# Performance work log

Hardware: AMD Instinct MI355X
Metric: run time of the kernel (lower is better)

Reference implementation:

```python
import jax, jax.numpy as jnp
import numpy as np

BATCH, SEQ_LEN, VEC_DIM, WIDTH = 64, 256, 512, 3


def setup_inputs() -> dict:
    key = jax.random.key(0)
    k = jax.random.split(key, 8)
    F0r = jax.random.normal(k[0], (BATCH, SEQ_LEN, VEC_DIM), jnp.float32)
    F1r = jax.random.normal(k[1], (BATCH, SEQ_LEN, VEC_DIM), jnp.float32)
    sent0_mask = (jax.random.uniform(k[2], (BATCH, SEQ_LEN)) < 0.9).astype(jnp.float32)
    sent1_mask = (jax.random.uniform(k[3], (BATCH, SEQ_LEN)) < 0.9).astype(jnp.float32)
    # nn.Parameter(torch.randn(seq_len, vec_dim))
    W0 = jax.random.normal(k[4], (SEQ_LEN, VEC_DIM), jnp.float32)
    W1 = jax.random.normal(k[5], (SEQ_LEN, VEC_DIM), jnp.float32)
    # Conv2d(2, 1, kernel_size=(WIDTH, 1)) default init: U(-1/sqrt(fan_in), +)
    bound = 1.0 / np.sqrt(2 * WIDTH * 1)
    conv_w = jax.random.uniform(k[6], (1, 2, WIDTH, 1), jnp.float32, -bound, bound)
    conv_b = jax.random.uniform(k[7], (1,), jnp.float32, -bound, bound)
    return dict(F0r=F0r, F1r=F1r, sent0_mask=sent0_mask, sent1_mask=sent1_mask,
                W0=W0, W1=W1, conv_w=conv_w, conv_b=conv_b)


def _conv_tanh_pool(x, conv_w, conv_b):
    # x: [B, 2, S, D]; conv pad (WIDTH-1, 0) -> [B, 1, S+WIDTH-1, D]
    y = jax.lax.conv_general_dilated(
        x, conv_w, window_strides=(1, 1),
        padding=((WIDTH - 1, WIDTH - 1), (0, 0)),
        dimension_numbers=('NCHW', 'OIHW', 'NCHW'))
    y = jnp.tanh(y + conv_b[None, :, None, None])
    # AvgPool2d kernel (WIDTH,1), stride 1 -> [B, 1, S, D]
    y = jax.lax.reduce_window(y, 0.0, jax.lax.add,
                              (1, 1, WIDTH, 1), (1, 1, 1, 1), 'VALID') / WIDTH
    return y[:, 0]  # squeeze channel -> [B, S, D]


def reference(F0r, F1r, sent0_mask, sent1_mask, W0, W1, conv_w, conv_b):
    # masking is in-place in the torch code, so masked F0/F1 feed the conv too
    F0 = F0r * sent0_mask[:, :, None]  # [B, S, D]
    F1 = F1r * sent1_mask[:, :, None]
    # pairwise L2 via ||u-v||^2 = ||u||^2 + ||v||^2 - 2 u.v (avoids [B,S,S,D])
    sq0 = jnp.sum(F0 * F0, axis=-1)  # [B, S]
    sq1 = jnp.sum(F1 * F1, axis=-1)
    cross = jnp.einsum('bid,bjd->bij', F0, F1)  # [B, S, S]
    d2 = jnp.maximum(sq0[:, :, None] + sq1[:, None, :] - 2.0 * cross, 0.0)
    norm = jnp.where(d2 > 0, jnp.sqrt(jnp.where(d2 > 0, d2, 1.0)), 0.0)
    A = 1.0 / (1.0 + norm)  # [B, S, S]
    F0a = jnp.einsum('bij,id->bjd', A, W0)  # A^T @ W0
    F1a = jnp.einsum('bij,jd->bid', A, W1)  # A @ W1
    x0 = jnp.stack([F0, F0a], axis=1)  # [B, 2, S, D]
    x1 = jnp.stack([F1, F1a], axis=1)
    out0 = _conv_tanh_pool(x0, conv_w, conv_b)
    out1 = _conv_tanh_pool(x1, conv_w, conv_b)
    return out0, out1
```

## Files before the change

### kernel.cpp

```cpp
#include <hip/hip_runtime.h>

typedef unsigned short u16;
typedef __attribute__((ext_vector_type(8))) short short8;
typedef __attribute__((ext_vector_type(4))) float f32x4;

__device__ inline u16 f2bf(float f) {
    union { float f; unsigned u; } v; v.f = f;
    unsigned u = v.u;
    unsigned r = (u + 0x7FFFu + ((u >> 16) & 1u)) >> 16;
    return (u16)r;
}
__device__ inline float bf2f(u16 h) {
    union { unsigned u; float f; } v; v.u = ((unsigned)h) << 16;
    return v.f;
}
__device__ inline float ftanh(float x) {
    float e = __expf(2.f * x);
    return 1.f - 2.f / (e + 1.f);
}

__global__ __launch_bounds__(128) void prep_kernel(
    const float* __restrict__ F0r, const float* __restrict__ F1r,
    const float* __restrict__ m0, const float* __restrict__ m1,
    const float* __restrict__ W0, const float* __restrict__ W1,
    u16* __restrict__ F0b, u16* __restrict__ F1b,
    u16* __restrict__ WT0, u16* __restrict__ WT1,
    float* __restrict__ sq0, float* __restrict__ sq1)
{
    int bx = blockIdx.x;
    int t = threadIdx.x;
    if (bx >= 16384) {
        int idx = (bx - 16384) * 128 + t;
        int a = idx >> 17;
        int r = idx & 131071;
        int s = r >> 9, d = r & 511;
        const float* W = a ? W1 : W0;
        u16* WT = a ? WT1 : WT0;
        WT[d * 256 + s] = f2bf(W[r]);
        return;
    }
    int bs = bx;
    size_t base = (size_t)bs * 512 + t * 4;
    float mk0 = m0[bs], mk1 = m1[bs];
    float4 v0 = *(const float4*)(F0r + base);
    float4 v1 = *(const float4*)(F1r + base);
    v0.x *= mk0; v0.y *= mk0; v0.z *= mk0; v0.w *= mk0;
    v1.x *= mk1; v1.y *= mk1; v1.z *= mk1; v1.w *= mk1;
    ushort4 u0; u0.x = f2bf(v0.x); u0.y = f2bf(v0.y); u0.z = f2bf(v0.z); u0.w = f2bf(v0.w);
    ushort4 u1; u1.x = f2bf(v1.x); u1.y = f2bf(v1.y); u1.z = f2bf(v1.z); u1.w = f2bf(v1.w);
    *(ushort4*)(F0b + base) = u0;
    *(ushort4*)(F1b + base) = u1;
    float s0p = v0.x*v0.x + v0.y*v0.y + v0.z*v0.z + v0.w*v0.w;
    float s1p = v1.x*v1.x + v1.y*v1.y + v1.z*v1.z + v1.w*v1.w;
    #pragma unroll
    for (int off = 32; off > 0; off >>= 1) {
        s0p += __shfl_xor(s0p, off);
        s1p += __shfl_xor(s1p, off);
    }
    __shared__ float red0[2], red1[2];
    if ((t & 63) == 0) { red0[t >> 6] = s0p; red1[t >> 6] = s1p; }
    __syncthreads();
    if (t == 0) { sq0[bs] = red0[0] + red0[1]; sq1[bs] = red1[0] + red1[1]; }
}

__global__ __launch_bounds__(256) void gemm_cross_kernel(
    const u16* __restrict__ F0b, const u16* __restrict__ F1b,
    const float* __restrict__ sq0, const float* __restrict__ sq1,
    u16* __restrict__ Abf, u16* __restrict__ ATbf)
{
    __shared__ __align__(16) u16 smem[64 * 136 * 2];
    u16 (*As)[136] = (u16(*)[136])smem;
    u16 (*Bs)[136] = (u16(*)[136])(smem + 64 * 136);

    int b = blockIdx.y;
    int i0 = (blockIdx.x >> 2) * 64, j0 = (blockIdx.x & 3) * 64;
    const u16* Ap = F0b + (size_t)b * 131072;
    const u16* Bp = F1b + (size_t)b * 131072;
    const float* sqR = sq0 + b * 256;
    const float* sqC = sq1 + b * 256;

    const int t = threadIdx.x;
    const int lane = t & 63, w = t >> 6;
    const int wm = w >> 1, wn = w & 1;
    const int q = lane >> 4, lm = lane & 15;

    f32x4 acc[2][2];
    #pragma unroll
    for (int x = 0; x < 2; ++x)
        #pragma unroll
        for (int y = 0; y < 2; ++y)
            acc[x][y] = (f32x4){0.f, 0.f, 0.f, 0.f};

    for (int k0 = 0; k0 < 512; k0 += 128) {
        #pragma unroll
        for (int i = 0; i < 4; ++i) {
            int idx = i * 256 + t;
            int row = idx >> 4;
            int seg = idx & 15;
            *(uint4*)&As[row][seg * 8] =
                *(const uint4*)(Ap + (size_t)(i0 + row) * 512 + k0 + seg * 8);
            *(uint4*)&Bs[row][seg * 8] =
                *(const uint4*)(Bp + (size_t)(j0 + row) * 512 + k0 + seg * 8);
        }
        __syncthreads();
        #pragma unroll
        for (int ks = 0; ks < 128; ks += 32) {
            short8 af[2], bfr[2];
            #pragma unroll
            for (int x = 0; x < 2; ++x) {
                af[x]  = *(const short8*)&As[wm * 32 + x * 16 + lm][ks + q * 8];
                bfr[x] = *(const short8*)&Bs[wn * 32 + x * 16 + lm][ks + q * 8];
            }
            #pragma unroll
            for (int x = 0; x < 2; ++x)
                #pragma unroll
                for (int y = 0; y < 2; ++y)
                    acc[x][y] = __builtin_amdgcn_mfma_f32_16x16x32_bf16(
                        af[x], bfr[y], acc[x][y], 0, 0, 0);
        }
        __syncthreads();
    }

    u16 (*Ct)[136] = (u16(*)[136])smem;
    #pragma unroll
    for (int x = 0; x < 2; ++x) {
        #pragma unroll
        for (int r = 0; r < 4; ++r) {
            int ir = wm * 32 + x * 16 + q * 4 + r;
            float si = sqR[i0 + ir];
            #pragma unroll
            for (int y = 0; y < 2; ++y) {
                int jc = wn * 32 + y * 16 + lm;
                float d2 = si + sqC[j0 + jc] - 2.f * acc[x][y][r];
                d2 = fmaxf(d2, 0.f);
                float a = 1.f / (1.f + sqrtf(d2));
                Ct[ir][jc] = f2bf(a);
            }
        }
    }
    __syncthreads();

    u16* Aout  = Abf  + (size_t)b * 65536;
    u16* ATout = ATbf + (size_t)b * 65536;
    int ii = t >> 2;
    int c0 = (t & 3) * 16;
    #pragma unroll
    for (int c = 0; c < 4; ++c) {
        ushort4 v = *(ushort4*)&Ct[ii][c0 + c * 4];
        *(ushort4*)&Aout[(size_t)(i0 + ii) * 256 + j0 + c0 + c * 4] = v;
    }
    #pragma unroll
    for (int c = 0; c < 4; ++c) {
        ushort4 v;
        v.x = Ct[c0 + c * 4 + 0][ii];
        v.y = Ct[c0 + c * 4 + 1][ii];
        v.z = Ct[c0 + c * 4 + 2][ii];
        v.w = Ct[c0 + c * 4 + 3][ii];
        *(ushort4*)&ATout[(size_t)(j0 + ii) * 256 + i0 + c0 + c * 4] = v;
    }
}

__global__ __launch_bounds__(256) void gemm_fa_kernel(
    const u16* __restrict__ Abf, const u16* __restrict__ ATbf,
    const u16* __restrict__ WT0, const u16* __restrict__ WT1,
    u16* __restrict__ F0a, u16* __restrict__ F1a)
{
    __shared__ __align__(16) u16 smem[64 * 72 + 128 * 72];
    u16 (*As)[72] = (u16(*)[72])smem;
    u16 (*Bs)[72] = (u16(*)[72])(smem + 64 * 72);

    int b = blockIdx.y, var = blockIdx.z;
    int m0 = (blockIdx.x >> 2) * 64;
    int n0 = (blockIdx.x & 3) * 128;
    const u16 *Ap, *Bp; u16* Out;
    if (var == 0) { Ap = ATbf + (size_t)b * 65536; Bp = WT0; Out = F0a + (size_t)b * 131072; }
    else          { Ap = Abf  + (size_t)b * 65536; Bp = WT1; Out = F1a + (size_t)b * 131072; }

    const int t = threadIdx.x;
    const int lane = t & 63, w = t >> 6;
    const int wm = w >> 1, wn = w & 1;
    const int q = lane >> 4, lm = lane & 15;

    f32x4 acc[2][4];
    #pragma unroll
    for (int x = 0; x < 2; ++x)
        #pragma unroll
        for (int y = 0; y < 4; ++y)
            acc[x][y] = (f32x4){0.f, 0.f, 0.f, 0.f};

    for (int k0 = 0; k0 < 256; k0 += 64) {
        #pragma unroll
        for (int i = 0; i < 6; ++i) {
            int idx = i * 256 + t;
            int row = idx >> 3;
            int seg = idx & 7;
            uint4 v;
            if (row < 64)
                v = *(const uint4*)(Ap + (size_t)(m0 + row) * 256 + k0 + seg * 8);
            else
                v = *(const uint4*)(Bp + (size_t)(n0 + row - 64) * 256 + k0 + seg * 8);
            if (row < 64) *(uint4*)&As[row][seg * 8] = v;
            else          *(uint4*)&Bs[row - 64][seg * 8] = v;
        }
        __syncthreads();
        #pragma unroll
        for (int ks = 0; ks < 64; ks += 32) {
            short8 af[2], bfr[4];
            #pragma unroll
            for (int x = 0; x < 2; ++x)
                af[x] = *(const short8*)&As[wm * 32 + x * 16 + lm][ks + q * 8];
            #pragma unroll
            for (int y = 0; y < 4; ++y)
                bfr[y] = *(const short8*)&Bs[wn * 64 + y * 16 + lm][ks + q * 8];
            #pragma unroll
            for (int x = 0; x < 2; ++x)
                #pragma unroll
                for (int y = 0; y < 4; ++y)
                    acc[x][y] = __builtin_amdgcn_mfma_f32_16x16x32_bf16(
                        af[x], bfr[y], acc[x][y], 0, 0, 0);
        }
        __syncthreads();
    }

    u16 (*Ct)[136] = (u16(*)[136])smem;
    #pragma unroll
    for (int x = 0; x < 2; ++x)
        #pragma unroll
        for (int r = 0; r < 4; ++r) {
            int ir = wm * 32 + x * 16 + q * 4 + r;
            #pragma unroll
            for (int y = 0; y < 4; ++y) {
                int jc = wn * 64 + y * 16 + lm;
                Ct[ir][jc] = f2bf(acc[x][y][r]);
            }
        }
    __syncthreads();
    int ii = t >> 2;
    int c0 = (t & 3) * 32;
    #pragma unroll
    for (int c = 0; c < 8; ++c) {
        ushort4 v = *(ushort4*)&Ct[ii][c0 + c * 4];
        *(ushort4*)&Out[(size_t)(m0 + ii) * 512 + n0 + c0 + c * 4] = v;
    }
}

__device__ inline void load_row_cv(
    const u16* __restrict__ Fb, const u16* __restrict__ Fa,
    int s, int d0, float4& f, float4& a)
{
    if ((unsigned)s < 256u) {
        ushort4 uf = *(const ushort4*)(Fb + (size_t)s * 512 + d0);
        ushort4 ua = *(const ushort4*)(Fa + (size_t)s * 512 + d0);
        f.x = bf2f(uf.x); f.y = bf2f(uf.y); f.z = bf2f(uf.z); f.w = bf2f(uf.w);
        a.x = bf2f(ua.x); a.y = bf2f(ua.y); a.z = bf2f(ua.z); a.w = bf2f(ua.w);
    } else {
        f = make_float4(0.f, 0.f, 0.f, 0.f);
        a = make_float4(0.f, 0.f, 0.f, 0.f);
    }
}

__global__ __launch_bounds__(128) void conv_kernel(
    const u16* __restrict__ F0b, const u16* __restrict__ F1b,
    const u16* __restrict__ F0a, const u16* __restrict__ F1a,
    const float* __restrict__ cw, const float* __restrict__ cb,
    float* __restrict__ out)
{
    int b = blockIdx.y;
    int which = blockIdx.z;
    int s0 = blockIdx.x * 16;
    int d0 = threadIdx.x * 4;
    const u16* Fb = (which ? F1b : F0b) + (size_t)b * 131072;
    const u16* Fa = (which ? F1a : F0a) + (size_t)b * 131072;
    float* o = out + (size_t)which * 8388608 + (size_t)b * 131072 + d0;
    float w00 = cw[0], w01 = cw[1], w02 = cw[2];
    float w10 = cw[3], w11 = cw[4], w12 = cw[5];
    float bias = cb[0];

    float4 fm2, fm1, fc, fp1, fp2, am2, am1, ac, ap1, ap2;
    load_row_cv(Fb, Fa, s0 - 2, d0, fm2, am2);
    load_row_cv(Fb, Fa, s0 - 1, d0, fm1, am1);
    load_row_cv(Fb, Fa, s0,     d0, fc,  ac);
    load_row_cv(Fb, Fa, s0 + 1, d0, fp1, ap1);
    load_row_cv(Fb, Fa, s0 + 2, d0, fp2, ap2);

    #define CONV_Y(Y, F0_, F1_, F2_, A0_, A1_, A2_)                                \
        { Y.x = bias + w00*F0_.x + w01*F1_.x + w02*F2_.x + w10*A0_.x + w11*A1_.x + w12*A2_.x; \
          Y.y = bias + w00*F0_.y + w01*F1_.y + w02*F2_.y + w10*A0_.y + w11*A1_.y + w12*A2_.y; \
          Y.z = bias + w00*F0_.z + w01*F1_.z + w02*F2_.z + w10*A0_.z + w11*A1_.z + w12*A2_.z; \
          Y.w = bias + w00*F0_.w + w01*F1_.w + w02*F2_.w + w10*A0_.w + w11*A1_.w + w12*A2_.w; }
    #define TANH4(Y) { Y.x = ftanh(Y.x); Y.y = ftanh(Y.y); Y.z = ftanh(Y.z); Y.w = ftanh(Y.w); }

    float4 ty0, ty1;
    CONV_Y(ty0, fm2, fm1, fc, am2, am1, ac); TANH4(ty0);
    CONV_Y(ty1, fm1, fc, fp1, am1, ac, ap1); TANH4(ty1);

    float4 w0f = fc, w1f = fp1, w2f = fp2;
    float4 w0a = ac, w1a = ap1, w2a = ap2;
    const float third = 1.f / 3.f;
    for (int s = s0; s < s0 + 16; ++s) {
        float4 ty2;
        CONV_Y(ty2, w0f, w1f, w2f, w0a, w1a, w2a); TANH4(ty2);
        float4 r;
        r.x = (ty0.x + ty1.x + ty2.x) * third;
        r.y = (ty0.y + ty1.y + ty2.y) * third;
        r.z = (ty0.z + ty1.z + ty2.z) * third;
        r.w = (ty0.w + ty1.w + ty2.w) * third;
        *(float4*)(o + (size_t)s * 512) = r;
        ty0 = ty1; ty1 = ty2;
        w0f = w1f; w1f = w2f;
        w0a = w1a; w1a = w2a;
        load_row_cv(Fb, Fa, s + 3, d0, w2f, w2a);
    }
    #undef CONV_Y
    #undef TANH4
}

extern "C" void kernel_launch(void* const* d_in, const int* in_sizes, int n_in,
                              void* d_out, int out_size, void* d_ws, size_t ws_size,
                              hipStream_t stream)
{
    const float* F0r = (const float*)d_in[0];
    const float* F1r = (const float*)d_in[1];
    const float* m0  = (const float*)d_in[2];
    const float* m1  = (const float*)d_in[3];
    const float* W0  = (const float*)d_in[4];
    const float* W1  = (const float*)d_in[5];
    const float* cw  = (const float*)d_in[6];
    const float* cb  = (const float*)d_in[7];
    float* out = (float*)d_out;

    char* ws = (char*)d_ws;
    u16* F0b   = (u16*)(ws);
    u16* F1b   = (u16*)(ws + 16777216);
    u16* F0a   = (u16*)(ws + 33554432);
    u16* F1a   = (u16*)(ws + 50331648);
    u16* Abf   = (u16*)(ws + 67108864);
    u16* ATbf  = (u16*)(ws + 75497472);
    float* sq0 = (float*)(ws + 83886080);
    float* sq1 = (float*)(ws + 83951616);
    u16* WT0   = (u16*)(ws + 84017152);
    u16* WT1   = (u16*)(ws + 84279296);

    prep_kernel<<<18432, 128, 0, stream>>>(F0r, F1r, m0, m1, W0, W1,
                                           F0b, F1b, WT0, WT1, sq0, sq1);
    gemm_cross_kernel<<<dim3(16, 64), 256, 0, stream>>>(F0b, F1b, sq0, sq1, Abf, ATbf);
    gemm_fa_kernel<<<dim3(16, 64, 2), 256, 0, stream>>>(Abf, ATbf, WT0, WT1, F0a, F1a);
    conv_kernel<<<dim3(16, 64, 2), 128, 0, stream>>>(F0b, F1b, F0a, F1a, cw, cb, out);
}
```

Baseline: 210.5 us.

## Fuse attention-weighted GEMM into conv/tanh/pool kernel with halo recompute

Merges the A·W GEMM that produced F0a/F1a into the convolution kernel: each block computes a 36-row halo tile of the GEMM output into shared memory, then applies the 3-tap conv, tanh and average pool directly. This removes the global write and re-read of the bf16 intermediates and one kernel launch. In exchange it recomputes halo rows, pads M to 48 rows, and uses more shared memory with a sequential loop over N chunks, which may reduce occupancy.

```diff
diff --git a/kernel.cpp b/kernel.cpp
--- a/kernel.cpp
+++ b/kernel.cpp
@@ -17,6 +17,10 @@
 __device__ inline float ftanh(float x) {
     float e = __expf(2.f * x);
     return 1.f - 2.f / (e + 1.f);
+}
+__device__ inline float4 bf4f(ushort4 u) {
+    float4 f; f.x = bf2f(u.x); f.y = bf2f(u.y); f.z = bf2f(u.z); f.w = bf2f(u.w);
+    return f;
 }
 
 __global__ __launch_bounds__(128) void prep_kernel(
@@ -160,159 +164,129 @@
     }
 }
 
-__global__ __launch_bounds__(256) void gemm_fa_kernel(
+__global__ __launch_bounds__(256) void fa_conv_kernel(
     const u16* __restrict__ Abf, const u16* __restrict__ ATbf,
     const u16* __restrict__ WT0, const u16* __restrict__ WT1,
-    u16* __restrict__ F0a, u16* __restrict__ F1a)
-{
-    __shared__ __align__(16) u16 smem[64 * 72 + 128 * 72];
-    u16 (*As)[72] = (u16(*)[72])smem;
-    u16 (*Bs)[72] = (u16(*)[72])(smem + 64 * 72);
-
-    int b = blockIdx.y, var = blockIdx.z;
-    int m0 = (blockIdx.x >> 2) * 64;
-    int n0 = (blockIdx.x & 3) * 128;
-    const u16 *Ap, *Bp; u16* Out;
-    if (var == 0) { Ap = ATbf + (size_t)b * 65536; Bp = WT0; Out = F0a + (size_t)b * 131072; }
-    else          { Ap = Abf  + (size_t)b * 65536; Bp = WT1; Out = F1a + (size_t)b * 131072; }
-
-    const int t = threadIdx.x;
-    const int lane = t & 63, w = t >> 6;
-    const int wm = w >> 1, wn = w & 1;
-    const int q = lane >> 4, lm = lane & 15;
-
-    f32x4 acc[2][4];
-    #pragma unroll
-    for (int x = 0; x < 2; ++x)
-        #pragma unroll
-        for (int y = 0; y < 4; ++y)
-            acc[x][y] = (f32x4){0.f, 0.f, 0.f, 0.f};
-
-    for (int k0 = 0; k0 < 256; k0 += 64) {
-        #pragma unroll
-        for (int i = 0; i < 6; ++i) {
-            int idx = i * 256 + t;
-            int row = idx >> 3;
-            int seg = idx & 7;
-            uint4 v;
-            if (row < 64)
-                v = *(const uint4*)(Ap + (size_t)(m0 + row) * 256 + k0 + seg * 8);
-            else
-                v = *(const uint4*)(Bp + (size_t)(n0 + row - 64) * 256 + k0 + seg * 8);
-            if (row < 64) *(uint4*)&As[row][seg * 8] = v;
-            else          *(uint4*)&Bs[row - 64][seg * 8] = v;
-        }
-        __syncthreads();
-        #pragma unroll
-        for (int ks = 0; ks < 64; ks += 32) {
-            short8 af[2], bfr[4];
-            #pragma unroll
-            for (int x = 0; x < 2; ++x)
-                af[x] = *(const short8*)&As[wm * 32 + x * 16 + lm][ks + q * 8];
-            #pragma unroll
-            for (int y = 0; y < 4; ++y)
-                bfr[y] = *(const short8*)&Bs[wn * 64 + y * 16 + lm][ks + q * 8];
-            #pragma unroll
-            for (int x = 0; x < 2; ++x)
-                #pragma unroll
-                for (int y = 0; y < 4; ++y)
-                    acc[x][y] = __builtin_amdgcn_mfma_f32_16x16x32_bf16(
-                        af[x], bfr[y], acc[x][y], 0, 0, 0);
-        }
-        __syncthreads();
-    }
-
-    u16 (*Ct)[136] = (u16(*)[136])smem;
-    #pragma unroll
-    for (int x = 0; x < 2; ++x)
-        #pragma unroll
-        for (int r = 0; r < 4; ++r) {
-            int ir = wm * 32 + x * 16 + q * 4 + r;
-            #pragma unroll
-            for (int y = 0; y < 4; ++y) {
-                int jc = wn * 64 + y * 16 + lm;
-                Ct[ir][jc] = f2bf(acc[x][y][r]);
-            }
-        }
-    __syncthreads();
-    int ii = t >> 2;
-    int c0 = (t & 3) * 32;
-    #pragma unroll
-    for (int c = 0; c < 8; ++c) {
-        ushort4 v = *(ushort4*)&Ct[ii][c0 + c * 4];
-        *(ushort4*)&Out[(size_t)(m0 + ii) * 512 + n0 + c0 + c * 4] = v;
-    }
-}
-
-__device__ inline void load_row_cv(
-    const u16* __restrict__ Fb, const u16* __restrict__ Fa,
-    int s, int d0, float4& f, float4& a)
-{
-    if ((unsigned)s < 256u) {
-        ushort4 uf = *(const ushort4*)(Fb + (size_t)s * 512 + d0);
-        ushort4 ua = *(const ushort4*)(Fa + (size_t)s * 512 + d0);
-        f.x = bf2f(uf.x); f.y = bf2f(uf.y); f.z = bf2f(uf.z); f.w = bf2f(uf.w);
-        a.x = bf2f(ua.x); a.y = bf2f(ua.y); a.z = bf2f(ua.z); a.w = bf2f(ua.w);
-    } else {
-        f = make_float4(0.f, 0.f, 0.f, 0.f);
-        a = make_float4(0.f, 0.f, 0.f, 0.f);
-    }
-}
-
-__global__ __launch_bounds__(128) void conv_kernel(
     const u16* __restrict__ F0b, const u16* __restrict__ F1b,
-    const u16* __restrict__ F0a, const u16* __restrict__ F1a,
     const float* __restrict__ cw, const float* __restrict__ cb,
     float* __restrict__ out)
 {
-    int b = blockIdx.y;
-    int which = blockIdx.z;
-    int s0 = blockIdx.x * 16;
-    int d0 = threadIdx.x * 4;
-    const u16* Fb = (which ? F1b : F0b) + (size_t)b * 131072;
-    const u16* Fa = (which ? F1a : F0a) + (size_t)b * 131072;
-    float* o = out + (size_t)which * 8388608 + (size_t)b * 131072 + d0;
+    __shared__ __align__(16) u16 Al[48][264];
+    __shared__ __align__(16) u16 Bl[128][72];
+    __shared__ __align__(16) u16 Fl[36][132];
+
+    int b = blockIdx.y, side = blockIdx.z;
+    int s0 = blockIdx.x * 32;
+    const u16* Ap = (side ? Abf : ATbf) + (size_t)b * 65536;
+    const u16* WT = side ? WT1 : WT0;
+    const u16* Fb = (side ? F1b : F0b) + (size_t)b * 131072;
+    float* o = out + (size_t)side * 8388608 + (size_t)b * 131072;
+
+    const int t = threadIdx.x;
+    const int lane = t & 63, w = t >> 6;
+    const int q = lane >> 4, lm = lane & 15;
+
+    #pragma unroll
+    for (int i = 0; i < 6; ++i) {
+        int idx = i * 256 + t;
+        int r = idx >> 5;
+        int seg = idx & 31;
+        int s = s0 - 2 + r;
+        uint4 v = {0u, 0u, 0u, 0u};
+        if (r < 36 && (unsigned)s < 256u)
+            v = *(const uint4*)(Ap + (size_t)s * 256 + seg * 8);
+        *(uint4*)&Al[r][seg * 8] = v;
+    }
+
     float w00 = cw[0], w01 = cw[1], w02 = cw[2];
     float w10 = cw[3], w11 = cw[4], w12 = cw[5];
     float bias = cb[0];
-
-    float4 fm2, fm1, fc, fp1, fp2, am2, am1, ac, ap1, ap2;
-    load_row_cv(Fb, Fa, s0 - 2, d0, fm2, am2);
-    load_row_cv(Fb, Fa, s0 - 1, d0, fm1, am1);
-    load_row_cv(Fb, Fa, s0,     d0, fc,  ac);
-    load_row_cv(Fb, Fa, s0 + 1, d0, fp1, ap1);
-    load_row_cv(Fb, Fa, s0 + 2, d0, fp2, ap2);
-
-    #define CONV_Y(Y, F0_, F1_, F2_, A0_, A1_, A2_)                                \
-        { Y.x = bias + w00*F0_.x + w01*F1_.x + w02*F2_.x + w10*A0_.x + w11*A1_.x + w12*A2_.x; \
-          Y.y = bias + w00*F0_.y + w01*F1_.y + w02*F2_.y + w10*A0_.y + w11*A1_.y + w12*A2_.y; \
-          Y.z = bias + w00*F0_.z + w01*F1_.z + w02*F2_.z + w10*A0_.z + w11*A1_.z + w12*A2_.z; \
-          Y.w = bias + w00*F0_.w + w01*F1_.w + w02*F2_.w + w10*A0_.w + w11*A1_.w + w12*A2_.w; }
-    #define TANH4(Y) { Y.x = ftanh(Y.x); Y.y = ftanh(Y.y); Y.z = ftanh(Y.z); Y.w = ftanh(Y.w); }
-
-    float4 ty0, ty1;
-    CONV_Y(ty0, fm2, fm1, fc, am2, am1, ac); TANH4(ty0);
-    CONV_Y(ty1, fm1, fc, fp1, am1, ac, ap1); TANH4(ty1);
-
-    float4 w0f = fc, w1f = fp1, w2f = fp2;
-    float4 w0a = ac, w1a = ap1, w2a = ap2;
     const float third = 1.f / 3.f;
-    for (int s = s0; s < s0 + 16; ++s) {
-        float4 ty2;
-        CONV_Y(ty2, w0f, w1f, w2f, w0a, w1a, w2a); TANH4(ty2);
-        float4 r;
-        r.x = (ty0.x + ty1.x + ty2.x) * third;
-        r.y = (ty0.y + ty1.y + ty2.y) * third;
-        r.z = (ty0.z + ty1.z + ty2.z) * third;
-        r.w = (ty0.w + ty1.w + ty2.w) * third;
-        *(float4*)(o + (size_t)s * 512) = r;
-        ty0 = ty1; ty1 = ty2;
-        w0f = w1f; w1f = w2f;
-        w0a = w1a; w1a = w2a;
-        load_row_cv(Fb, Fa, s + 3, d0, w2f, w2a);
-    }
-    #undef CONV_Y
-    #undef TANH4
+    const int g = t >> 5;
+    const int dl = (t & 31) * 4;
+
+    for (int n0 = 0; n0 < 512; n0 += 128) {
+        f32x4 acc[3][2];
+        #pragma unroll
+        for (int x = 0; x < 3; ++x)
+            #pragma unroll
+            for (int y = 0; y < 2; ++y)
+                acc[x][y] = (f32x4){0.f, 0.f, 0.f, 0.f};
+
+        for (int kb = 0; kb < 256; kb += 64) {
+            #pragma unroll
+            for (int i = 0; i < 4; ++i) {
+                int idx = i * 256 + t;
+                int r = idx >> 3;
+                int seg = idx & 7;
+                *(uint4*)&Bl[r][seg * 8] =
+                    *(const uint4*)(WT + (size_t)(n0 + r) * 256 + kb + seg * 8);
+            }
+            __syncthreads();
+            #pragma unroll
+            for (int ks = 0; ks < 64; ks += 32) {
+                short8 af[3], bfr[2];
+                #pragma unroll
+                for (int x = 0; x < 3; ++x)
+                    af[x] = *(const short8*)&Al[x * 16 + lm][kb + ks + q * 8];
+                #pragma unroll
+                for (int y = 0; y < 2; ++y)
+                    bfr[y] = *(const short8*)&Bl[w * 32 + y * 16 + lm][ks + q * 8];
+                #pragma unroll
+                for (int x = 0; x < 3; ++x)
+                    #pragma unroll
+                    for (int y = 0; y < 2; ++y)
+                        acc[x][y] = __builtin_amdgcn_mfma_f32_16x16x32_bf16(
+                            af[x], bfr[y], acc[x][y], 0, 0, 0);
+            }
+            __syncthreads();
+        }
+
+        #pragma unroll
+        for (int x = 0; x < 3; ++x)
+            #pragma unroll
+            for (int r = 0; r < 4; ++r) {
+                int m = x * 16 + q * 4 + r;
+                if (m < 36) {
+                    #pragma unroll
+                    for (int y = 0; y < 2; ++y)
+                        Fl[m][w * 32 + y * 16 + lm] = f2bf(acc[x][y][r]);
+                }
+            }
+        __syncthreads();
+
+        float4 f[8], a[8];
+        #pragma unroll
+        for (int k = 0; k < 8; ++k) {
+            int s = s0 + g * 4 - 2 + k;
+            if ((unsigned)s < 256u)
+                f[k] = bf4f(*(const ushort4*)(Fb + (size_t)s * 512 + n0 + dl));
+            else
+                f[k] = make_float4(0.f, 0.f, 0.f, 0.f);
+            a[k] = bf4f(*(const ushort4*)&Fl[g * 4 + k][dl]);
+        }
+        float4 ty[6];
+        #pragma unroll
+        for (int k = 0; k < 6; ++k) {
+            float4 y;
+            y.x = bias + w00*f[k].x + w01*f[k+1].x + w02*f[k+2].x + w10*a[k].x + w11*a[k+1].x + w12*a[k+2].x;
+            y.y = bias + w00*f[k].y + w01*f[k+1].y + w02*f[k+2].y + w10*a[k].y + w11*a[k+1].y + w12*a[k+2].y;
+            y.z = bias + w00*f[k].z + w01*f[k+1].z + w02*f[k+2].z + w10*a[k].z + w11*a[k+1].z + w12*a[k+2].z;
+            y.w = bias + w00*f[k].w + w01*f[k+1].w + w02*f[k+2].w + w10*a[k].w + w11*a[k+1].w + w12*a[k+2].w;
+            y.x = ftanh(y.x); y.y = ftanh(y.y); y.z = ftanh(y.z); y.w = ftanh(y.w);
+            ty[k] = y;
+        }
+        #pragma unroll
+        for (int r = 0; r < 4; ++r) {
+            float4 res;
+            res.x = (ty[r].x + ty[r+1].x + ty[r+2].x) * third;
+            res.y = (ty[r].y + ty[r+1].y + ty[r+2].y) * third;
+            res.z = (ty[r].z + ty[r+1].z + ty[r+2].z) * third;
+            res.w = (ty[r].w + ty[r+1].w + ty[r+2].w) * third;
+            *(float4*)(o + (size_t)(s0 + g * 4 + r) * 512 + n0 + dl) = res;
+        }
+        __syncthreads();
+    }
 }
 
 extern "C" void kernel_launch(void* const* d_in, const int* in_sizes, int n_in,
@@ -332,18 +306,16 @@
     char* ws = (char*)d_ws;
     u16* F0b   = (u16*)(ws);
     u16* F1b   = (u16*)(ws + 16777216);
-    u16* F0a   = (u16*)(ws + 33554432);
-    u16* F1a   = (u16*)(ws + 50331648);
-    u16* Abf   = (u16*)(ws + 67108864);
-    u16* ATbf  = (u16*)(ws + 75497472);
-    float* sq0 = (float*)(ws + 83886080);
-    float* sq1 = (float*)(ws + 83951616);
-    u16* WT0   = (u16*)(ws + 84017152);
-    u16* WT1   = (u16*)(ws + 84279296);
+    u16* Abf   = (u16*)(ws + 33554432);
+    u16* ATbf  = (u16*)(ws + 41943040);
+    float* sq0 = (float*)(ws + 50331648);
+    float* sq1 = (float*)(ws + 50397184);
+    u16* WT0   = (u16*)(ws + 50462720);
+    u16* WT1   = (u16*)(ws + 50724864);
 
     prep_kernel<<<18432, 128, 0, stream>>>(F0r, F1r, m0, m1, W0, W1,
                                            F0b, F1b, WT0, WT1, sq0, sq1);
     gemm_cross_kernel<<<dim3(16, 64), 256, 0, stream>>>(F0b, F1b, sq0, sq1, Abf, ATbf);
-    gemm_fa_kernel<<<dim3(16, 64, 2), 256, 0, stream>>>(Abf, ATbf, WT0, WT1, F0a, F1a);
-    conv_kernel<<<dim3(16, 64, 2), 128, 0, stream>>>(F0b, F1b, F0a, F1a, cw, cb, out);
-}
+    fa_conv_kernel<<<dim3(8, 64, 2), 256, 0, stream>>>(Abf, ATbf, WT0, WT1,
+                                                       F0b, F1b, cw, cb, out);
+}
```

Result: faster. 201.4 us (-4.3%).
